# Kernel optimization log

Hardware: AMD Instinct MI355X
Metric: run time of the kernel (lower is better)

## Reference

```python
import jax, jax.numpy as jnp
import numpy as np

NQ = 4   # num_qubits (CNOT chain in source hardcodes wires 0..3)
NL = 1   # num_layers
B = 1048576

# CNOT as rank-4 tensor [c_out, t_out, c_in, t_in]
_CNOT = jnp.asarray(
    np.array([[1, 0, 0, 0],
              [0, 1, 0, 0],
              [0, 0, 0, 1],
              [0, 0, 1, 0]], dtype=np.complex64).reshape(2, 2, 2, 2))


def _rz(t):
    e = jnp.exp(-0.5j * t.astype(jnp.complex64))
    z = jnp.zeros_like(e)
    return jnp.stack([jnp.stack([e, z]), jnp.stack([z, jnp.conj(e)])])


def _ry(t):
    c = jnp.cos(0.5 * t).astype(jnp.complex64)
    s = jnp.sin(0.5 * t).astype(jnp.complex64)
    return jnp.stack([jnp.stack([c, -s]), jnp.stack([s, c])])


def _u3(th, ph, lm):
    c = jnp.cos(0.5 * th).astype(jnp.complex64)
    s = jnp.sin(0.5 * th).astype(jnp.complex64)
    eph = jnp.exp(1j * ph.astype(jnp.complex64))
    elm = jnp.exp(1j * lm.astype(jnp.complex64))
    return jnp.stack([jnp.stack([c, -elm * s]),
                      jnp.stack([eph * s, eph * elm * c])])


def _apply_1q(state, U, q):
    s = jnp.tensordot(U, state, axes=([1], [q]))
    return jnp.moveaxis(s, 0, q)


def _apply_2q(state, U, c, t):
    s = jnp.tensordot(U, state, axes=([2, 3], [c, t]))
    return jnp.moveaxis(s, (0, 1), (c, t))


def _circuit(enc, w):
    # H on all qubits applied to |0...0> -> uniform real amplitude 2^{-NQ/2}
    state = jnp.full((2,) * NQ, 2.0 ** (-NQ / 2), dtype=jnp.complex64)
    # per-qubit encoding: RZ, RY, RZ
    for q in range(NQ):
        state = _apply_1q(state, _rz(enc[q, 0]), q)
        state = _apply_1q(state, _ry(enc[q, 1]), q)
        state = _apply_1q(state, _rz(enc[q, 2]), q)
    for l in range(NL):
        for (c, t) in ((0, 1), (1, 2), (2, 3), (3, 0)):
            state = _apply_2q(state, _CNOT, c, t)
        for q in range(NQ):
            state = _apply_1q(state, _u3(w[l, q, 0], w[l, q, 1], w[l, q, 2]), q)
    probs = jnp.real(state * jnp.conj(state))
    zs = []
    for q in range(NQ):
        p = probs.sum(axis=tuple(i for i in range(NQ) if i != q))  # (2,)
        zs.append(p[0] - p[1])
    return jnp.stack(zs)  # (NQ,)


def setup_inputs() -> dict:
    key = jax.random.key(0)
    k1, k2 = jax.random.split(key)
    enc_angles = jax.random.normal(k1, (B, NQ, 3), dtype=jnp.float32)
    weights = jax.random.normal(k2, (NL, NQ, 3), dtype=jnp.float32)
    return {"enc_angles": enc_angles, "weights": weights}


def reference(enc_angles, weights):
    out = jax.vmap(lambda e: _circuit(e, weights))(enc_angles)  # (B, NQ)
    return out.astype(jnp.float32)
```

## Files before the change

### kernel.cpp

```cpp
#include <hip/hip_runtime.h>


__global__ void vqc_prep(const float* __restrict__ w, float* __restrict__ mz) {
    int q = threadIdx.x;
    if (q >= 4) return;
    float th = w[q * 3 + 0];
    float lm = w[q * 3 + 2];
    float s, c, sl, cl;
    sincosf(0.5f * th, &s, &c);
    sincosf(lm, &sl, &cl);
    mz[q * 4 + 0] = c * c - s * s;
    mz[q * 4 + 1] = -4.0f * c * s * cl;
    mz[q * 4 + 2] = -4.0f * c * s * sl;
    mz[q * 4 + 3] = 0.0f;
}

__global__ __launch_bounds__(256) void vqc_main(const float4* __restrict__ enc,
                                                const float4* __restrict__ mz,
                                                float4* __restrict__ out, int B) {
    int b = blockIdx.x * blockDim.x + threadIdx.x;
    if (b >= B) return;

    float4 e0 = enc[b * 3 + 0];
    float4 e1 = enc[b * 3 + 1];
    float4 e2 = enc[b * 3 + 2];
    float4 m0 = mz[0], m1 = mz[1], m2 = mz[2], m3 = mz[3];

    float ang[12] = {e0.x, e0.y, e0.z, e0.w, e1.x, e1.y, e1.z, e1.w,
                     e2.x, e2.y, e2.z, e2.w};

    float vx[4][2], vy[4][2];
    const float inv = 0.70710678118654752f;
#pragma unroll
    for (int q = 0; q < 4; ++q) {
        float sa, ca, sb, cb, sg, cg;
        __sincosf(0.5f * ang[3 * q + 0], &sa, &ca);
        __sincosf(0.5f * ang[3 * q + 1], &sb, &cb);
        __sincosf(0.5f * ang[3 * q + 2], &sg, &cg);
        float P = cb - sb, Q = cb + sb;
        float y0x = ca * P * inv, y0y = -sa * Q * inv;
        float y1x = ca * Q * inv, y1y = sa * P * inv;
        vx[q][0] = cg * y0x + sg * y0y;
        vy[q][0] = cg * y0y - sg * y0x;
        vx[q][1] = cg * y1x - sg * y1y;
        vy[q][1] = cg * y1y + sg * y1x;
    }

    float ux[4], uy[4], wx[4], wy[4];
#pragma unroll
    for (int i = 0; i < 2; ++i)
#pragma unroll
        for (int j = 0; j < 2; ++j) {
            ux[i * 2 + j] = vx[0][i] * vx[1][j] - vy[0][i] * vy[1][j];
            uy[i * 2 + j] = vx[0][i] * vy[1][j] + vy[0][i] * vx[1][j];
            wx[i * 2 + j] = vx[2][i] * vx[3][j] - vy[2][i] * vy[3][j];
            wy[i * 2 + j] = vx[2][i] * vy[3][j] + vy[2][i] * vx[3][j];
        }

    float ax[16], ay[16];
#pragma unroll
    for (int h = 0; h < 4; ++h)
#pragma unroll
        for (int l = 0; l < 4; ++l) {
            ax[h * 4 + l] = ux[h] * wx[l] - uy[h] * wy[l];
            ay[h * 4 + l] = ux[h] * wy[l] + uy[h] * wx[l];
        }

    const int cm[4] = {8, 4, 2, 1};
    const int tm[4] = {4, 2, 1, 8};
#pragma unroll
    for (int k = 0; k < 4; ++k) {
#pragma unroll
        for (int i = 0; i < 16; ++i) {
            if ((i & cm[k]) && !(i & tm[k])) {
                int j = i | tm[k];
                float tx = ax[i], ty = ay[i];
                ax[i] = ax[j]; ay[i] = ay[j];
                ax[j] = tx;    ay[j] = ty;
            }
        }
    }

    float p[16];
#pragma unroll
    for (int i = 0; i < 16; ++i) p[i] = ax[i] * ax[i] + ay[i] * ay[i];

    float al[4] = {m0.x, m1.x, m2.x, m3.x};
    float g1[4] = {m0.y, m1.y, m2.y, m3.y};
    float g2[4] = {m0.z, m1.z, m2.z, m3.z};

    float z[4];
#pragma unroll
    for (int q = 0; q < 4; ++q) {
        int m = 8 >> q;
        float acc = 0.0f;
#pragma unroll
        for (int i = 0; i < 16; ++i) {
            if (!(i & m)) {
                int j = i | m;
                float cx = ax[i] * ax[j] + ay[i] * ay[j];
                float cy = ay[i] * ax[j] - ax[i] * ay[j];
                acc += al[q] * (p[i] - p[j]) + g1[q] * cx + g2[q] * cy;
            }
        }
        z[q] = acc;
    }

    out[b] = make_float4(z[0], z[1], z[2], z[3]);
}

extern "C" void kernel_launch(void* const* d_in, const int* in_sizes, int n_in,
                              void* d_out, int out_size, void* d_ws, size_t ws_size,
                              hipStream_t stream) {
    const float* enc = (const float*)d_in[0];
    const float* w   = (const float*)d_in[1];
    float* out = (float*)d_out;
    float* mz  = (float*)d_ws;

    int B = in_sizes[0] / 12;

    vqc_prep<<<1, 64, 0, stream>>>(w, mz);
    int grid = (B + 255) / 256;
    vqc_main<<<grid, 256, 0, stream>>>((const float4*)enc, (const float4*)mz,
                                       (float4*)out, B);
}
```

Measured before the change: 92.62 us.

## Fuse weight prep into main kernel and stage angle loads through LDS

Removes the separate single-block prep kernel by having each block compute the four per-qubit weight coefficients into shared memory, which saves one launch and the dependency between the two kernels. Encoding angles are now loaded coalesced into LDS (three float4 per thread, contiguous across threads) and then read back per thread, instead of each thread issuing strided float4 loads. The cost is a __syncthreads, 12KB of LDS per block that may limit occupancy, LDS bank conflicts on the stride-3 float4 reads, and redundant weight trig in every block.

```diff
diff --git a/kernel.cpp b/kernel.cpp
--- a/kernel.cpp
+++ b/kernel.cpp
@@ -1,31 +1,39 @@
 #include <hip/hip_runtime.h>
 
 
-__global__ void vqc_prep(const float* __restrict__ w, float* __restrict__ mz) {
-    int q = threadIdx.x;
-    if (q >= 4) return;
-    float th = w[q * 3 + 0];
-    float lm = w[q * 3 + 2];
-    float s, c, sl, cl;
-    sincosf(0.5f * th, &s, &c);
-    sincosf(lm, &sl, &cl);
-    mz[q * 4 + 0] = c * c - s * s;
-    mz[q * 4 + 1] = -4.0f * c * s * cl;
-    mz[q * 4 + 2] = -4.0f * c * s * sl;
-    mz[q * 4 + 3] = 0.0f;
-}
+__global__ __launch_bounds__(256) void vqc_fused(const float4* __restrict__ enc,
+                                                 const float* __restrict__ w,
+                                                 float4* __restrict__ out, int B) {
+    __shared__ float4 stage[768];
+    __shared__ float4 wc[4];
 
-__global__ __launch_bounds__(256) void vqc_main(const float4* __restrict__ enc,
-                                                const float4* __restrict__ mz,
-                                                float4* __restrict__ out, int B) {
-    int b = blockIdx.x * blockDim.x + threadIdx.x;
+    const int tid  = threadIdx.x;
+    const int base = blockIdx.x * 256;
+    const long gbase = (long)base * 3;
+
+#pragma unroll
+    for (int k = 0; k < 3; ++k) {
+        long gi = gbase + tid + 256 * k;
+        if (gi < (long)B * 3) stage[tid + 256 * k] = enc[gi];
+    }
+
+    if (tid < 4) {
+        const int q = tid;
+        float th = w[q * 3 + 0];
+        float lm = w[q * 3 + 2];
+        float s, c, sl, cl;
+        __sincosf(0.5f * th, &s, &c);
+        __sincosf(lm, &sl, &cl);
+        wc[q] = make_float4(c * c - s * s, -4.0f * c * s * cl, -4.0f * c * s * sl, 0.0f);
+    }
+    __syncthreads();
+
+    const int b = base + tid;
     if (b >= B) return;
 
-    float4 e0 = enc[b * 3 + 0];
-    float4 e1 = enc[b * 3 + 1];
-    float4 e2 = enc[b * 3 + 2];
-    float4 m0 = mz[0], m1 = mz[1], m2 = mz[2], m3 = mz[3];
-
+    float4 e0 = stage[3 * tid + 0];
+    float4 e1 = stage[3 * tid + 1];
+    float4 e2 = stage[3 * tid + 2];
     float ang[12] = {e0.x, e0.y, e0.z, e0.w, e1.x, e1.y, e1.z, e1.w,
                      e2.x, e2.y, e2.z, e2.w};
 
@@ -46,15 +54,15 @@
         vy[q][1] = cg * y1y + sg * y1x;
     }
 
-    float ux[4], uy[4], wx[4], wy[4];
+    float ux[4], uy[4], wxx[4], wyy[4];
 #pragma unroll
     for (int i = 0; i < 2; ++i)
 #pragma unroll
         for (int j = 0; j < 2; ++j) {
-            ux[i * 2 + j] = vx[0][i] * vx[1][j] - vy[0][i] * vy[1][j];
-            uy[i * 2 + j] = vx[0][i] * vy[1][j] + vy[0][i] * vx[1][j];
-            wx[i * 2 + j] = vx[2][i] * vx[3][j] - vy[2][i] * vy[3][j];
-            wy[i * 2 + j] = vx[2][i] * vy[3][j] + vy[2][i] * vx[3][j];
+            ux[i * 2 + j]  = vx[0][i] * vx[1][j] - vy[0][i] * vy[1][j];
+            uy[i * 2 + j]  = vx[0][i] * vy[1][j] + vy[0][i] * vx[1][j];
+            wxx[i * 2 + j] = vx[2][i] * vx[3][j] - vy[2][i] * vy[3][j];
+            wyy[i * 2 + j] = vx[2][i] * vy[3][j] + vy[2][i] * vx[3][j];
         }
 
     float ax[16], ay[16];
@@ -62,8 +70,8 @@
     for (int h = 0; h < 4; ++h)
 #pragma unroll
         for (int l = 0; l < 4; ++l) {
-            ax[h * 4 + l] = ux[h] * wx[l] - uy[h] * wy[l];
-            ay[h * 4 + l] = ux[h] * wy[l] + uy[h] * wx[l];
+            ax[h * 4 + l] = ux[h] * wxx[l] - uy[h] * wyy[l];
+            ay[h * 4 + l] = ux[h] * wyy[l] + uy[h] * wxx[l];
         }
 
     const int cm[4] = {8, 4, 2, 1};
@@ -85,9 +93,10 @@
 #pragma unroll
     for (int i = 0; i < 16; ++i) p[i] = ax[i] * ax[i] + ay[i] * ay[i];
 
-    float al[4] = {m0.x, m1.x, m2.x, m3.x};
-    float g1[4] = {m0.y, m1.y, m2.y, m3.y};
-    float g2[4] = {m0.z, m1.z, m2.z, m3.z};
+    float4 w0 = wc[0], w1 = wc[1], w2 = wc[2], w3 = wc[3];
+    float al[4] = {w0.x, w1.x, w2.x, w3.x};
+    float g1[4] = {w0.y, w1.y, w2.y, w3.y};
+    float g2[4] = {w0.z, w1.z, w2.z, w3.z};
 
     float z[4];
 #pragma unroll
@@ -115,12 +124,8 @@
     const float* enc = (const float*)d_in[0];
     const float* w   = (const float*)d_in[1];
     float* out = (float*)d_out;
-    float* mz  = (float*)d_ws;
 
     int B = in_sizes[0] / 12;
-
-    vqc_prep<<<1, 64, 0, stream>>>(w, mz);
     int grid = (B + 255) / 256;
-    vqc_main<<<grid, 256, 0, stream>>>((const float4*)enc, (const float4*)mz,
-                                       (float4*)out, B);
+    vqc_fused<<<grid, 256, 0, stream>>>((const float4*)enc, w, (float4*)out, B);
 }
```

Result: no change. 92.78 us (+0.2%).
